# Performance work log

Measured on AMD Instinct MI355X. Metric: run time of the kernel, lower is better.

The kernel has to match this reference:

```python
import jax, jax.numpy as jnp
import numpy as np

D = 1024
H = 16
HD = D // H
MLP = 4 * D


def _lin(key, fin, fout):
    k1, k2 = jax.random.split(key)
    lim = 1.0 / np.sqrt(fin)
    W = jax.random.uniform(k1, (fin, fout), minval=-lim, maxval=lim, dtype=jnp.float32)
    b = jax.random.uniform(k2, (fout,), minval=-lim, maxval=lim, dtype=jnp.float32)
    return W, b


def setup_inputs() -> dict:
    key = jax.random.key(0)
    ks = jax.random.split(key, 10)
    x = jax.random.normal(ks[0], (4, 2048, D), dtype=jnp.float32)
    time_emb = jax.random.normal(ks[1], (4, D), dtype=jnp.float32)
    Wqkv, bqkv = _lin(ks[2], D, 3 * D)
    Wproj, bproj = _lin(ks[3], D, D)
    W1, b1 = _lin(ks[4], D, MLP)
    W2, b2 = _lin(ks[5], MLP, D)
    Wt, bt = _lin(ks[6], D, 6 * D)
    g1 = jnp.ones((D,), jnp.float32); be1 = jnp.zeros((D,), jnp.float32)
    g2 = jnp.ones((D,), jnp.float32); be2 = jnp.zeros((D,), jnp.float32)
    return {"x": x, "time_emb": time_emb, "Wqkv": Wqkv, "bqkv": bqkv,
            "Wproj": Wproj, "bproj": bproj, "W1": W1, "b1": b1, "W2": W2, "b2": b2,
            "Wt": Wt, "bt": bt, "g1": g1, "be1": be1, "g2": g2, "be2": be2}


def layernorm(x, g, b, eps=1e-5):
    mu = jnp.mean(x, axis=-1, keepdims=True)
    var = jnp.var(x, axis=-1, keepdims=True)
    return (x - mu) * jax.lax.rsqrt(var + eps) * g + b


def attention(h, Wqkv, bqkv, Wproj, bproj):
    B, L, _ = h.shape
    qkv = (h @ Wqkv + bqkv).reshape(B, L, 3, H, HD)
    q, k, v = jnp.moveaxis(qkv, 2, 0)  # each [B,L,H,HD]
    scale = HD ** -0.5
    attn = jnp.einsum('blhd,bmhd->bhlm', q, k) * scale
    attn = jax.nn.softmax(attn, axis=-1)
    out = jnp.einsum('bhlm,bmhd->blhd', attn, v).reshape(B, L, D)
    return out @ Wproj + bproj


def reference(x, time_emb, Wqkv, bqkv, Wproj, bproj, W1, b1, W2, b2, Wt, bt, g1, be1, g2, be2):
    tp = (jax.nn.silu(time_emb) @ Wt + bt)[:, None, :]  # [B,1,6D]
    shift_msa, scale_msa, gate_msa, shift_mlp, scale_mlp, gate_mlp = jnp.split(tp, 6, axis=-1)
    h = layernorm(x, g1, be1)
    h = h * (1.0 + scale_msa) + shift_msa
    h = attention(h, Wqkv, bqkv, Wproj, bproj)
    x = x + gate_msa * h
    h = layernorm(x, g2, be2)
    h = h * (1.0 + scale_mlp) + shift_mlp
    h = jax.nn.gelu(h @ W1 + b1, approximate=False) @ W2 + b2
    x = x + gate_mlp * h
    return x
```

## Files before the change

### kernel.cpp

```cpp
#include <hip/hip_runtime.h>
#include <hip/hip_bf16.h>
#include <math.h>


typedef __attribute__((ext_vector_type(8))) __bf16 bf16x8;
typedef __attribute__((ext_vector_type(4))) float f32x4;

union FragU { uint4 u; bf16x8 b; };

#define AS1(p) ((const __attribute__((address_space(1))) void*)(p))
#define AS3(p) ((__attribute__((address_space(3))) void*)(p))

__device__ __forceinline__ float bflo(uint u) {
    union { uint i; float f; } v; v.i = u << 16; return v.f;
}
__device__ __forceinline__ ushort f2bf(float f) {
    union { float f; uint i; } v; v.f = f;
    uint r = (v.i + 0x7fffu + ((v.i >> 16) & 1u)) >> 16;
    return (ushort)r;
}
__device__ __forceinline__ uint pkbf(float a, float b) {
    return __builtin_amdgcn_perm(__float_as_uint(b), __float_as_uint(a), 0x07060302u);
}
__device__ __forceinline__ void stval(ushort* p, float v) { *p = f2bf(v); }
__device__ __forceinline__ void stval(float* p, float v) { *p = v; }

__global__ __launch_bounds__(256) void transpose_f2b(const float* __restrict__ in,
                                                     ushort* __restrict__ out,
                                                     int R, int C) {
    __shared__ ushort t[32][33];
    int c0 = blockIdx.x * 32, r0 = blockIdx.y * 32;
    int tx = threadIdx.x, ty = threadIdx.y;
#pragma unroll
    for (int i = 0; i < 32; i += 8)
        t[ty + i][tx] = f2bf(in[(size_t)(r0 + ty + i) * C + c0 + tx]);
    __syncthreads();
#pragma unroll
    for (int i = 0; i < 32; i += 8)
        out[(size_t)(c0 + ty + i) * R + r0 + tx] = t[tx][ty + i];
}

__global__ __launch_bounds__(256) void tp_gemm(const float* __restrict__ te,
                                               const ushort* __restrict__ WtT,
                                               const float* __restrict__ bt,
                                               float* __restrict__ tp) {
    int w = blockIdx.x * 4 + (threadIdx.x >> 6);
    int lane = threadIdx.x & 63;
    int b = w / 6144, n = w % 6144;
    const ushort* wr = WtT + (size_t)n * 1024;
    const float* tr = te + (size_t)b * 1024;
    float s = 0.f;
#pragma unroll
    for (int i = 0; i < 16; i++) {
        int k = lane + 64 * i;
        float t = tr[k];
        float sil = t / (1.f + __expf(-t));
        s += sil * bflo((uint)wr[k]);
    }
#pragma unroll
    for (int x = 32; x; x >>= 1) s += __shfl_xor(s, x);
    if (lane == 0) tp[(size_t)b * 6144 + n] = s + bt[n];
}

__global__ __launch_bounds__(256) void ln_mod(const float* __restrict__ x,
                                              const float* __restrict__ tpb,
                                              const float* __restrict__ g,
                                              const float* __restrict__ be,
                                              ushort* __restrict__ out,
                                              int shift_off, int scale_off) {
    __shared__ float2 sred[4];
    int row = blockIdx.x;
    int b = row >> 11;
    int tid = threadIdx.x;
    float4 f = *(const float4*)&x[(size_t)row * 1024 + tid * 4];
    float v[4] = {f.x, f.y, f.z, f.w};
    float s = v[0] + v[1] + v[2] + v[3];
    float s2 = v[0] * v[0] + v[1] * v[1] + v[2] * v[2] + v[3] * v[3];
#pragma unroll
    for (int m = 32; m; m >>= 1) { s += __shfl_xor(s, m); s2 += __shfl_xor(s2, m); }
    if ((tid & 63) == 0) sred[tid >> 6] = make_float2(s, s2);
    __syncthreads();
    s = sred[0].x + sred[1].x + sred[2].x + sred[3].x;
    s2 = sred[0].y + sred[1].y + sred[2].y + sred[3].y;
    float mu = s * (1.f / 1024.f);
    float var = s2 * (1.f / 1024.f) - mu * mu;
    float rs = rsqrtf(var + 1e-5f);
    const float* tprow = tpb + (size_t)b * 6144;
    ushort o4[4];
#pragma unroll
    for (int t = 0; t < 4; t++) {
        int c = tid * 4 + t;
        float y = (v[t] - mu) * rs * g[c] + be[c];
        y = y * (1.f + tprow[scale_off + c]) + tprow[shift_off + c];
        o4[t] = f2bf(y);
    }
    *(uint2*)&out[(size_t)row * 1024 + tid * 4] = *(uint2*)o4;
}

template <int EPI, typename OT>
__global__ __launch_bounds__(256) void gemm_bt(const ushort* __restrict__ A,
                                               const ushort* __restrict__ BT,
                                               const float* __restrict__ bias,
                                               OT* __restrict__ C,
                                               int M, int N, int K,
                                               const float* __restrict__ res,
                                               const float* __restrict__ tpb,
                                               int goff) {
    __shared__ __align__(16) ushort As[128 * 32];
    __shared__ __align__(16) ushort Bs[128 * 32];
    int m0 = blockIdx.y * 128, n0 = blockIdx.x * 128;
    int tid = threadIdx.x;
    int wid = tid >> 6, lane = tid & 63;
    int wy = wid >> 1, wx = wid & 1;
    int r16 = lane & 15;
    int q8 = (lane >> 4) << 3;

    f32x4 acc[4][4];
#pragma unroll
    for (int i = 0; i < 4; i++)
#pragma unroll
        for (int j = 0; j < 4; j++) acc[i][j] = (f32x4){0.f, 0.f, 0.f, 0.f};

    int sr = tid >> 2;
    int sc = (tid & 3) << 3;
    const ushort* Abase = A + (size_t)(m0 + sr) * K + sc;
    const ushort* Bbase = BT + (size_t)(n0 + sr) * K + sc;
    ushort* AsW = As + (size_t)wid * 512;
    ushort* BsW = Bs + (size_t)wid * 512;

    for (int k0 = 0; k0 < K; k0 += 32) {
        __builtin_amdgcn_global_load_lds(AS1(Abase + k0), AS3(AsW), 16, 0, 0);
        __builtin_amdgcn_global_load_lds(AS1(Abase + (size_t)64 * K + k0), AS3(AsW + 2048), 16, 0, 0);
        __builtin_amdgcn_global_load_lds(AS1(Bbase + k0), AS3(BsW), 16, 0, 0);
        __builtin_amdgcn_global_load_lds(AS1(Bbase + (size_t)64 * K + k0), AS3(BsW + 2048), 16, 0, 0);
        __syncthreads();
        FragU fa[4], fb[4];
#pragma unroll
        for (int i = 0; i < 4; i++)
            fa[i].u = *(const uint4*)&As[(wy * 64 + i * 16 + r16) * 32 + q8];
#pragma unroll
        for (int j = 0; j < 4; j++)
            fb[j].u = *(const uint4*)&Bs[(wx * 64 + j * 16 + r16) * 32 + q8];
#pragma unroll
        for (int i = 0; i < 4; i++)
#pragma unroll
            for (int j = 0; j < 4; j++)
                acc[i][j] = __builtin_amdgcn_mfma_f32_16x16x32_bf16(fa[i].b, fb[j].b, acc[i][j], 0, 0, 0);
        __syncthreads();
    }

    int q4 = (lane >> 4) << 2;
#pragma unroll
    for (int i = 0; i < 4; i++) {
#pragma unroll
        for (int j = 0; j < 4; j++) {
            int col = n0 + wx * 64 + j * 16 + r16;
            float bv = bias[col];
#pragma unroll
            for (int t = 0; t < 4; t++) {
                int row = m0 + wy * 64 + i * 16 + q4 + t;
                float v = acc[i][j][t] + bv;
                if constexpr (EPI == 1) {
                    v = 0.5f * v * (1.f + erff(v * 0.70710678118f));
                }
                if constexpr (EPI == 2) {
                    float rv = res[(size_t)row * N + col];
                    float gate = tpb[(size_t)(row >> 11) * 6144 + goff + col];
                    v = rv + gate * v;
                }
                stval(&C[(size_t)row * N + col], v);
            }
        }
    }
}

__global__ __launch_bounds__(256, 4) void attn_mfma(const ushort* __restrict__ qkv,
                                                    ushort* __restrict__ out) {
    __shared__ __align__(16) ushort Ks[64 * 72];
    __shared__ __align__(16) ushort Vs[64 * 72];
    __shared__ __align__(16) ushort Ps[64 * 72];

    int tid = threadIdx.x;
    int wid = tid >> 6, lane = tid & 63;
    int r16 = lane & 15, quad = lane >> 4;
    int q8 = quad << 3, q4 = quad << 2;

    int bh = blockIdx.x >> 5;
    int qt = blockIdx.x & 31;
    int b = bh >> 4, h = bh & 15;
    const ushort* qkbase = qkv + (size_t)b * 2048 * 3072 + h * 64;

    {
        int r = tid >> 2;
        int c = (tid & 3) << 4;
        const ushort* qp = qkbase + (size_t)(qt * 64 + r) * 3072 + c;
        *(uint4*)&Ps[r * 72 + c] = *(const uint4*)qp;
        *(uint4*)&Ps[r * 72 + c + 8] = *(const uint4*)(qp + 8);
    }
    __syncthreads();
    FragU qa[2];
#pragma unroll
    for (int ks = 0; ks < 2; ks++)
        qa[ks].u = *(const uint4*)&Ps[(wid * 16 + r16) * 72 + ks * 32 + q8];

    float m_ = -1e30f, l_ = 0.f;
    f32x4 o[4];
#pragma unroll
    for (int dn = 0; dn < 4; dn++) o[dn] = (f32x4){0.f, 0.f, 0.f, 0.f};

    int kr = tid >> 2;
    int kc = (tid & 3) << 4;
    int vk = (tid & 31) << 1;
    int vd = (tid >> 5) << 3;
    const ushort* kptr = qkbase + 1024 + (size_t)kr * 3072 + kc;
    const ushort* vptr = qkbase + 2048 + (size_t)vk * 3072 + vd;

    uint4 ka0 = *(const uint4*)kptr;
    uint4 ka1 = *(const uint4*)(kptr + 8);
    uint4 va0 = *(const uint4*)vptr;
    uint4 va1 = *(const uint4*)(vptr + 3072);

    for (int kt = 0; kt < 32; kt++) {
        __syncthreads();
        *(uint4*)&Ks[kr * 72 + kc] = ka0;
        *(uint4*)&Ks[kr * 72 + kc + 8] = ka1;
        *(uint*)&Vs[(vd + 0) * 72 + vk] = (va0.x & 0xffffu) | (va1.x << 16);
        *(uint*)&Vs[(vd + 1) * 72 + vk] = (va0.x >> 16) | (va1.x & 0xffff0000u);
        *(uint*)&Vs[(vd + 2) * 72 + vk] = (va0.y & 0xffffu) | (va1.y << 16);
        *(uint*)&Vs[(vd + 3) * 72 + vk] = (va0.y >> 16) | (va1.y & 0xffff0000u);
        *(uint*)&Vs[(vd + 4) * 72 + vk] = (va0.z & 0xffffu) | (va1.z << 16);
        *(uint*)&Vs[(vd + 5) * 72 + vk] = (va0.z >> 16) | (va1.z & 0xffff0000u);
        *(uint*)&Vs[(vd + 6) * 72 + vk] = (va0.w & 0xffffu) | (va1.w << 16);
        *(uint*)&Vs[(vd + 7) * 72 + vk] = (va0.w >> 16) | (va1.w & 0xffff0000u);
        __syncthreads();

        if (kt < 31) {
            const ushort* kp2 = kptr + (size_t)(kt + 1) * 64 * 3072;
            const ushort* vp2 = vptr + (size_t)(kt + 1) * 64 * 3072;
            ka0 = *(const uint4*)kp2;
            ka1 = *(const uint4*)(kp2 + 8);
            va0 = *(const uint4*)vp2;
            va1 = *(const uint4*)(vp2 + 3072);
        }

        f32x4 s[4];
#pragma unroll
        for (int n = 0; n < 4; n++) s[n] = (f32x4){0.f, 0.f, 0.f, 0.f};
#pragma unroll
        for (int ks = 0; ks < 2; ks++) {
            FragU kb[4];
#pragma unroll
            for (int n = 0; n < 4; n++)
                kb[n].u = *(const uint4*)&Ks[(n * 16 + r16) * 72 + ks * 32 + q8];
#pragma unroll
            for (int n = 0; n < 4; n++)
                s[n] = __builtin_amdgcn_mfma_f32_16x16x32_bf16(kb[n].b, qa[ks].b, s[n], 0, 0, 0);
        }

        float mx = fmaxf(fmaxf(fmaxf(s[0][0], s[0][1]), fmaxf(s[0][2], s[0][3])),
                         fmaxf(fmaxf(s[1][0], s[1][1]), fmaxf(s[1][2], s[1][3])));
        mx = fmaxf(mx, fmaxf(fmaxf(fmaxf(s[2][0], s[2][1]), fmaxf(s[2][2], s[2][3])),
                             fmaxf(fmaxf(s[3][0], s[3][1]), fmaxf(s[3][2], s[3][3]))));
        mx = fmaxf(mx, __shfl_xor(mx, 16));
        mx = fmaxf(mx, __shfl_xor(mx, 32));
        float nm = fmaxf(m_, mx);
        float al = __expf((m_ - nm) * 0.125f);
        float cc = nm * 0.125f;
        m_ = nm;

        float p[4][4];
        float ps = 0.f;
#pragma unroll
        for (int n = 0; n < 4; n++)
#pragma unroll
            for (int t = 0; t < 4; t++) {
                p[n][t] = __expf(__fmaf_rn(s[n][t], 0.125f, -cc));
                ps += p[n][t];
            }
        ps += __shfl_xor(ps, 16);
        ps += __shfl_xor(ps, 32);
        l_ = l_ * al + ps;
#pragma unroll
        for (int dn = 0; dn < 4; dn++)
#pragma unroll
            for (int t = 0; t < 4; t++) o[dn][t] *= al;

#pragma unroll
        for (int n = 0; n < 4; n++) {
            uint2 w2 = make_uint2(pkbf(p[n][0], p[n][1]), pkbf(p[n][2], p[n][3]));
            *(uint2*)&Ps[(wid * 16 + r16) * 72 + n * 16 + q4] = w2;
        }

#pragma unroll
        for (int ks = 0; ks < 2; ks++) {
            FragU pa, vb[4];
            pa.u = *(const uint4*)&Ps[(wid * 16 + r16) * 72 + ks * 32 + q8];
#pragma unroll
            for (int dn = 0; dn < 4; dn++)
                vb[dn].u = *(const uint4*)&Vs[(dn * 16 + r16) * 72 + ks * 32 + q8];
#pragma unroll
            for (int dn = 0; dn < 4; dn++)
                o[dn] = __builtin_amdgcn_mfma_f32_16x16x32_bf16(vb[dn].b, pa.b, o[dn], 0, 0, 0);
        }
    }

    float inv = 1.f / l_;
    int row = qt * 64 + wid * 16 + r16;
    ushort* orow = out + (size_t)(b * 2048 + row) * 1024 + h * 64;
#pragma unroll
    for (int dn = 0; dn < 4; dn++) {
        uint2 w2 = make_uint2(pkbf(o[dn][0] * inv, o[dn][1] * inv),
                              pkbf(o[dn][2] * inv, o[dn][3] * inv));
        *(uint2*)&orow[dn * 16 + q4] = w2;
    }
}

extern "C" void kernel_launch(void* const* d_in, const int* in_sizes, int n_in,
                              void* d_out, int out_size, void* d_ws, size_t ws_size,
                              hipStream_t stream) {
    const float* x    = (const float*)d_in[0];
    const float* te   = (const float*)d_in[1];
    const float* Wqkv = (const float*)d_in[2];
    const float* bqkv = (const float*)d_in[3];
    const float* Wproj= (const float*)d_in[4];
    const float* bproj= (const float*)d_in[5];
    const float* W1   = (const float*)d_in[6];
    const float* b1   = (const float*)d_in[7];
    const float* W2   = (const float*)d_in[8];
    const float* b2   = (const float*)d_in[9];
    const float* Wt   = (const float*)d_in[10];
    const float* bt   = (const float*)d_in[11];
    const float* g1   = (const float*)d_in[12];
    const float* be1  = (const float*)d_in[13];
    const float* g2   = (const float*)d_in[14];
    const float* be2  = (const float*)d_in[15];

    char* ws = (char*)d_ws;
    ushort* WqkvT  = (ushort*)(ws + 0);
    ushort* WprojT = (ushort*)(ws + 6291456);
    ushort* W1T    = (ushort*)(ws + 8388608);
    ushort* W2T    = (ushort*)(ws + 16777216);
    ushort* WtT    = (ushort*)(ws + 25165824);
    float*  tpb    = (float*)(ws + 37748736);
    ushort* hbuf   = (ushort*)(ws + 37847040);
    ushort* qkvb   = (ushort*)(ws + 54624256);
    ushort* midb   = (ushort*)(ws + 54624256);
    ushort* attnb  = (ushort*)(ws + 121733120);
    float*  x1b    = (float*)(ws + 138510336);

    dim3 tb(32, 8);
    hipLaunchKernelGGL(transpose_f2b, dim3(3072 / 32, 1024 / 32), tb, 0, stream, Wqkv, WqkvT, 1024, 3072);
    hipLaunchKernelGGL(transpose_f2b, dim3(1024 / 32, 1024 / 32), tb, 0, stream, Wproj, WprojT, 1024, 1024);
    hipLaunchKernelGGL(transpose_f2b, dim3(4096 / 32, 1024 / 32), tb, 0, stream, W1, W1T, 1024, 4096);
    hipLaunchKernelGGL(transpose_f2b, dim3(1024 / 32, 4096 / 32), tb, 0, stream, W2, W2T, 4096, 1024);
    hipLaunchKernelGGL(transpose_f2b, dim3(6144 / 32, 1024 / 32), tb, 0, stream, Wt, WtT, 1024, 6144);

    hipLaunchKernelGGL(tp_gemm, dim3(6144), dim3(256), 0, stream, te, WtT, bt, tpb);

    hipLaunchKernelGGL(ln_mod, dim3(8192), dim3(256), 0, stream, x, tpb, g1, be1, hbuf, 0, 1024);

    hipLaunchKernelGGL((gemm_bt<0, ushort>), dim3(3072 / 128, 8192 / 128), dim3(256), 0, stream,
                       hbuf, WqkvT, bqkv, qkvb, 8192, 3072, 1024, (const float*)nullptr, (const float*)nullptr, 0);

    hipLaunchKernelGGL(attn_mfma, dim3(2048), dim3(256), 0, stream, qkvb, attnb);

    hipLaunchKernelGGL((gemm_bt<2, float>), dim3(1024 / 128, 8192 / 128), dim3(256), 0, stream,
                       attnb, WprojT, bproj, x1b, 8192, 1024, 1024, x, tpb, 2048);

    hipLaunchKernelGGL(ln_mod, dim3(8192), dim3(256), 0, stream, x1b, tpb, g2, be2, hbuf, 3072, 4096);

    hipLaunchKernelGGL((gemm_bt<1, ushort>), dim3(4096 / 128, 8192 / 128), dim3(256), 0, stream,
                       hbuf, W1T, b1, midb, 8192, 4096, 1024, (const float*)nullptr, (const float*)nullptr, 0);

    hipLaunchKernelGGL((gemm_bt<2, float>), dim3(1024 / 128, 8192 / 128), dim3(256), 0, stream,
                       midb, W2T, b2, (float*)d_out, 8192, 1024, 4096, x1b, tpb, 5120);
}
```

Baseline: 674.1 us.

## Double K-step in GEMM, pre-transpose V, use exp2 softmax and tanh GELU

The GEMM main loop now stages two 32-wide K slices per barrier pair, halving the number of __syncthreads. A separate kernel writes V transposed per head into the freed hbuf region, so attention can load V with straight vector stores instead of a scattered transpose into LDS. The softmax switches to exp2f with a pre-folded log2e scale. The exact erf GELU is replaced by the tanh approximation, which changes the numerics relative to the reference.

```diff
diff --git a/kernel.cpp b/kernel.cpp
--- a/kernel.cpp
+++ b/kernel.cpp
@@ -13,6 +13,9 @@
 
 __device__ __forceinline__ float bflo(uint u) {
     union { uint i; float f; } v; v.i = u << 16; return v.f;
+}
+__device__ __forceinline__ float bfhi(uint u) {
+    union { uint i; float f; } v; v.i = u & 0xffff0000u; return v.f;
 }
 __device__ __forceinline__ ushort f2bf(float f) {
     union { float f; uint i; } v; v.f = f;
@@ -24,6 +27,13 @@
 }
 __device__ __forceinline__ void stval(ushort* p, float v) { *p = f2bf(v); }
 __device__ __forceinline__ void stval(float* p, float v) { *p = v; }
+
+__device__ __forceinline__ float gelu_f(float x) {
+    float y = 0.7978845608f * (x + 0.044715f * x * x * x);
+    float e = exp2f(y * 2.88539008178f);
+    float t = 1.f - 2.f / (1.f + e);
+    return 0.5f * x * (1.f + t);
+}
 
 __global__ __launch_bounds__(256) void transpose_f2b(const float* __restrict__ in,
                                                      ushort* __restrict__ out,
@@ -38,6 +48,22 @@
 #pragma unroll
     for (int i = 0; i < 32; i += 8)
         out[(size_t)(c0 + ty + i) * R + r0 + tx] = t[tx][ty + i];
+}
+
+__global__ __launch_bounds__(256) void transpose_v(const ushort* __restrict__ qkv,
+                                                   ushort* __restrict__ vT) {
+    int bh = blockIdx.x >> 5, lt = blockIdx.x & 31;
+    int b = bh >> 4, h = bh & 15;
+    int d = threadIdx.x & 63, lg = threadIdx.x >> 6;
+    const ushort* src = qkv + (size_t)b * 2048 * 3072 + 2048 + h * 64 + d;
+#pragma unroll
+    for (int g = 0; g < 2; g++) {
+        int l0 = lt * 64 + lg * 16 + g * 8;
+        ushort v[8];
+#pragma unroll
+        for (int i = 0; i < 8; i++) v[i] = src[(size_t)(l0 + i) * 3072];
+        *(uint4*)&vT[((size_t)bh * 64 + d) * 2048 + l0] = *(uint4*)v;
+    }
 }
 
 __global__ __launch_bounds__(256) void tp_gemm(const float* __restrict__ te,
@@ -106,8 +132,8 @@
                                                const float* __restrict__ res,
                                                const float* __restrict__ tpb,
                                                int goff) {
-    __shared__ __align__(16) ushort As[128 * 32];
-    __shared__ __align__(16) ushort Bs[128 * 32];
+    __shared__ __align__(16) ushort As[2][128 * 32];
+    __shared__ __align__(16) ushort Bs[2][128 * 32];
     int m0 = blockIdx.y * 128, n0 = blockIdx.x * 128;
     int tid = threadIdx.x;
     int wid = tid >> 6, lane = tid & 63;
@@ -125,27 +151,34 @@
     int sc = (tid & 3) << 3;
     const ushort* Abase = A + (size_t)(m0 + sr) * K + sc;
     const ushort* Bbase = BT + (size_t)(n0 + sr) * K + sc;
-    ushort* AsW = As + (size_t)wid * 512;
-    ushort* BsW = Bs + (size_t)wid * 512;
-
-    for (int k0 = 0; k0 < K; k0 += 32) {
-        __builtin_amdgcn_global_load_lds(AS1(Abase + k0), AS3(AsW), 16, 0, 0);
-        __builtin_amdgcn_global_load_lds(AS1(Abase + (size_t)64 * K + k0), AS3(AsW + 2048), 16, 0, 0);
-        __builtin_amdgcn_global_load_lds(AS1(Bbase + k0), AS3(BsW), 16, 0, 0);
-        __builtin_amdgcn_global_load_lds(AS1(Bbase + (size_t)64 * K + k0), AS3(BsW + 2048), 16, 0, 0);
+
+    for (int k0 = 0; k0 < K; k0 += 64) {
+#pragma unroll
+        for (int c = 0; c < 2; c++) {
+            ushort* AsW = As[c] + wid * 512;
+            ushort* BsW = Bs[c] + wid * 512;
+            int kk = k0 + 32 * c;
+            __builtin_amdgcn_global_load_lds(AS1(Abase + kk), AS3(AsW), 16, 0, 0);
+            __builtin_amdgcn_global_load_lds(AS1(Abase + (size_t)64 * K + kk), AS3(AsW + 2048), 16, 0, 0);
+            __builtin_amdgcn_global_load_lds(AS1(Bbase + kk), AS3(BsW), 16, 0, 0);
+            __builtin_amdgcn_global_load_lds(AS1(Bbase + (size_t)64 * K + kk), AS3(BsW + 2048), 16, 0, 0);
+        }
         __syncthreads();
-        FragU fa[4], fb[4];
-#pragma unroll
-        for (int i = 0; i < 4; i++)
-            fa[i].u = *(const uint4*)&As[(wy * 64 + i * 16 + r16) * 32 + q8];
-#pragma unroll
-        for (int j = 0; j < 4; j++)
-            fb[j].u = *(const uint4*)&Bs[(wx * 64 + j * 16 + r16) * 32 + q8];
-#pragma unroll
-        for (int i = 0; i < 4; i++)
+#pragma unroll
+        for (int c = 0; c < 2; c++) {
+            FragU fa[4], fb[4];
+#pragma unroll
+            for (int i = 0; i < 4; i++)
+                fa[i].u = *(const uint4*)&As[c][(wy * 64 + i * 16 + r16) * 32 + q8];
 #pragma unroll
             for (int j = 0; j < 4; j++)
-                acc[i][j] = __builtin_amdgcn_mfma_f32_16x16x32_bf16(fa[i].b, fb[j].b, acc[i][j], 0, 0, 0);
+                fb[j].u = *(const uint4*)&Bs[c][(wx * 64 + j * 16 + r16) * 32 + q8];
+#pragma unroll
+            for (int i = 0; i < 4; i++)
+#pragma unroll
+                for (int j = 0; j < 4; j++)
+                    acc[i][j] = __builtin_amdgcn_mfma_f32_16x16x32_bf16(fa[i].b, fb[j].b, acc[i][j], 0, 0, 0);
+        }
         __syncthreads();
     }
 
@@ -161,7 +194,7 @@
                 int row = m0 + wy * 64 + i * 16 + q4 + t;
                 float v = acc[i][j][t] + bv;
                 if constexpr (EPI == 1) {
-                    v = 0.5f * v * (1.f + erff(v * 0.70710678118f));
+                    v = gelu_f(v);
                 }
                 if constexpr (EPI == 2) {
                     float rv = res[(size_t)row * N + col];
@@ -175,6 +208,7 @@
 }
 
 __global__ __launch_bounds__(256, 4) void attn_mfma(const ushort* __restrict__ qkv,
+                                                    const ushort* __restrict__ vT,
                                                     ushort* __restrict__ out) {
     __shared__ __align__(16) ushort Ks[64 * 72];
     __shared__ __align__(16) ushort Vs[64 * 72];
@@ -189,6 +223,7 @@
     int qt = blockIdx.x & 31;
     int b = bh >> 4, h = bh & 15;
     const ushort* qkbase = qkv + (size_t)b * 2048 * 3072 + h * 64;
+    const float SC = 0.18033688011f;
 
     {
         int r = tid >> 2;
@@ -210,37 +245,29 @@
 
     int kr = tid >> 2;
     int kc = (tid & 3) << 4;
-    int vk = (tid & 31) << 1;
-    int vd = (tid >> 5) << 3;
     const ushort* kptr = qkbase + 1024 + (size_t)kr * 3072 + kc;
-    const ushort* vptr = qkbase + 2048 + (size_t)vk * 3072 + vd;
+    const ushort* vptr = vT + (size_t)bh * 131072 + (size_t)kr * 2048 + kc;
 
     uint4 ka0 = *(const uint4*)kptr;
     uint4 ka1 = *(const uint4*)(kptr + 8);
     uint4 va0 = *(const uint4*)vptr;
-    uint4 va1 = *(const uint4*)(vptr + 3072);
+    uint4 va1 = *(const uint4*)(vptr + 8);
 
     for (int kt = 0; kt < 32; kt++) {
         __syncthreads();
         *(uint4*)&Ks[kr * 72 + kc] = ka0;
         *(uint4*)&Ks[kr * 72 + kc + 8] = ka1;
-        *(uint*)&Vs[(vd + 0) * 72 + vk] = (va0.x & 0xffffu) | (va1.x << 16);
-        *(uint*)&Vs[(vd + 1) * 72 + vk] = (va0.x >> 16) | (va1.x & 0xffff0000u);
-        *(uint*)&Vs[(vd + 2) * 72 + vk] = (va0.y & 0xffffu) | (va1.y << 16);
-        *(uint*)&Vs[(vd + 3) * 72 + vk] = (va0.y >> 16) | (va1.y & 0xffff0000u);
-        *(uint*)&Vs[(vd + 4) * 72 + vk] = (va0.z & 0xffffu) | (va1.z << 16);
-        *(uint*)&Vs[(vd + 5) * 72 + vk] = (va0.z >> 16) | (va1.z & 0xffff0000u);
-        *(uint*)&Vs[(vd + 6) * 72 + vk] = (va0.w & 0xffffu) | (va1.w << 16);
-        *(uint*)&Vs[(vd + 7) * 72 + vk] = (va0.w >> 16) | (va1.w & 0xffff0000u);
+        *(uint4*)&Vs[kr * 72 + kc] = va0;
+        *(uint4*)&Vs[kr * 72 + kc + 8] = va1;
         __syncthreads();
 
         if (kt < 31) {
             const ushort* kp2 = kptr + (size_t)(kt + 1) * 64 * 3072;
-            const ushort* vp2 = vptr + (size_t)(kt + 1) * 64 * 3072;
+            const ushort* vp2 = vptr + (kt + 1) * 64;
             ka0 = *(const uint4*)kp2;
             ka1 = *(const uint4*)(kp2 + 8);
             va0 = *(const uint4*)vp2;
-            va1 = *(const uint4*)(vp2 + 3072);
+            va1 = *(const uint4*)(vp2 + 8);
         }
 
         f32x4 s[4];
@@ -264,8 +291,8 @@
         mx = fmaxf(mx, __shfl_xor(mx, 16));
         mx = fmaxf(mx, __shfl_xor(mx, 32));
         float nm = fmaxf(m_, mx);
-        float al = __expf((m_ - nm) * 0.125f);
-        float cc = nm * 0.125f;
+        float al = exp2f((m_ - nm) * SC);
+        float cc = nm * SC;
         m_ = nm;
 
         float p[4][4];
@@ -274,7 +301,7 @@
         for (int n = 0; n < 4; n++)
 #pragma unroll
             for (int t = 0; t < 4; t++) {
-                p[n][t] = __expf(__fmaf_rn(s[n][t], 0.125f, -cc));
+                p[n][t] = exp2f(__fmaf_rn(s[n][t], SC, -cc));
                 ps += p[n][t];
             }
         ps += __shfl_xor(ps, 16);
@@ -343,6 +370,7 @@
     ushort* WtT    = (ushort*)(ws + 25165824);
     float*  tpb    = (float*)(ws + 37748736);
     ushort* hbuf   = (ushort*)(ws + 37847040);
+    ushort* vTb    = (ushort*)(ws + 37847040);
     ushort* qkvb   = (ushort*)(ws + 54624256);
     ushort* midb   = (ushort*)(ws + 54624256);
     ushort* attnb  = (ushort*)(ws + 121733120);
@@ -362,7 +390,9 @@
     hipLaunchKernelGGL((gemm_bt<0, ushort>), dim3(3072 / 128, 8192 / 128), dim3(256), 0, stream,
                        hbuf, WqkvT, bqkv, qkvb, 8192, 3072, 1024, (const float*)nullptr, (const float*)nullptr, 0);
 
-    hipLaunchKernelGGL(attn_mfma, dim3(2048), dim3(256), 0, stream, qkvb, attnb);
+    hipLaunchKernelGGL(transpose_v, dim3(2048), dim3(256), 0, stream, qkvb, vTb);
+
+    hipLaunchKernelGGL(attn_mfma, dim3(2048), dim3(256), 0, stream, qkvb, vTb, attnb);
 
     hipLaunchKernelGGL((gemm_bt<2, float>), dim3(1024 / 128, 8192 / 128), dim3(256), 0, stream,
                        attnb, WprojT, bproj, x1b, 8192, 1024, 1024, x, tpb, 2048);
```

Result: no change. 666.8 us (-1.1%).
